# Performance work log

Hardware: AMD Instinct MI355X
Metric: run time of the kernel (lower is better)

The kernel has to match this reference:

```python
import math
import jax, jax.numpy as jnp
import numpy as np

LAM = 1.0
TAU = 0.5
MOM = 0.1
INV_LAM = 1.0 / LAM
E = math.e


def lambertw0(z):
    """Principal branch W0(z) for z >= -1/e via series init + Halley iterations."""
    # init near branch point -1/e: W0 ~ -1 + p - p^2/3 + 11 p^3/72, p = sqrt(2(e z + 1))
    p = jnp.sqrt(jnp.maximum(2.0 * (E * z + 1.0), 0.0))
    w_small = -1.0 + p * (1.0 + p * (-1.0 / 3.0 + p * (11.0 / 72.0)))
    w_big = jnp.log1p(z)  # decent init for z >= 0
    w = jnp.where(z < 0.25, w_small, w_big)
    for _ in range(6):  # Halley's method, quadratic+ convergence
        ew = jnp.exp(w)
        f = w * ew - z
        wp1 = w + 1.0
        denom = ew * wp1 - (w + 2.0) * f / (2.0 * wp1)
        w = w - f / denom
    return w


def setup_inputs() -> dict:
    key = jax.random.key(0)
    loss = jax.random.uniform(key, (33554432,), dtype=jnp.float32)
    return {"loss": loss}


def reference(loss):
    # compute_sigma operates on detached loss -> stop_gradient
    l = jax.lax.stop_gradient(loss)
    tau = (1.0 - MOM) * TAU + MOM * jnp.mean(l)  # running-average tau update
    beta = (l - tau) * INV_LAM
    z = 0.5 * jnp.maximum(-2.0 * math.exp(-1.0), beta)
    sigma = jnp.exp(-lambertw0(z))
    superloss = sigma * loss
    return superloss, sigma
```

## Files before the change

### kernel.cpp

```cpp
#include <hip/hip_runtime.h>


#define NEG_2_OVER_E (-0.73575888234288464320f)

__global__ void __launch_bounds__(256) sum_kernel(const float* __restrict__ loss,
                                                  double* __restrict__ sum_out, int n) {
    int tid = blockIdx.x * blockDim.x + threadIdx.x;
    int stride = gridDim.x * blockDim.x;
    const float4* l4 = (const float4*)loss;
    int n4 = n >> 2;
    float s = 0.0f;
    for (int i = tid; i < n4; i += stride) {
        float4 v = l4[i];
        s += (v.x + v.y) + (v.z + v.w);
    }
    #pragma unroll
    for (int off = 32; off > 0; off >>= 1)
        s += __shfl_down(s, off, 64);
    __shared__ float wsum[4];
    int lane = threadIdx.x & 63;
    int wave = threadIdx.x >> 6;
    if (lane == 0) wsum[wave] = s;
    __syncthreads();
    if (threadIdx.x == 0) {
        float tot = (wsum[0] + wsum[1]) + (wsum[2] + wsum[3]);
        atomicAdd(sum_out, (double)tot);
    }
}

__device__ __forceinline__ float w0_fast(float z) {
    float w = z * fmaf(z, fmaf(z, fmaf(z, fmaf(z, 5.2083333f, -2.6666667f),
                                       1.5f), -1.0f), 1.0f);
    #pragma unroll
    for (int it = 0; it < 2; ++it) {
        float ew = __expf(w);
        float f = fmaf(w, ew, -z);
        float wp1 = w + 1.0f;
        float denom = fmaf(2.0f * ew, wp1 * wp1, -(w + 2.0f) * f);
        w = fmaf(-2.0f * f * wp1, __builtin_amdgcn_rcpf(denom), w);
    }
    return w;
}

__device__ __forceinline__ float sigma_of(float l, float tau) {
    float beta = l - tau;
    float z = 0.5f * fmaxf(NEG_2_OVER_E, beta);
    return __expf(-w0_fast(z));
}

__global__ void __launch_bounds__(256) superloss_kernel(const float* __restrict__ loss,
                                                        float* __restrict__ out,
                                                        const double* __restrict__ sum_ptr,
                                                        int n) {
    int i = blockIdx.x * blockDim.x + threadIdx.x;
    int n4 = n >> 2;
    if (i >= n4) return;

    float mean = (float)(*sum_ptr) * (1.0f / 33554432.0f);
    if (n != 33554432) mean = (float)(*sum_ptr) / (float)n;
    float tau = fmaf(0.1f, mean, 0.45f);

    const float4* l4 = (const float4*)loss;
    float4* sl4 = (float4*)out;
    float4* sg4 = (float4*)(out + n);

    float4 l = l4[i];
    float4 sg, sl;
    sg.x = sigma_of(l.x, tau);
    sg.y = sigma_of(l.y, tau);
    sg.z = sigma_of(l.z, tau);
    sg.w = sigma_of(l.w, tau);
    sl.x = sg.x * l.x;
    sl.y = sg.y * l.y;
    sl.z = sg.z * l.z;
    sl.w = sg.w * l.w;
    sl4[i] = sl;
    sg4[i] = sg;
}

extern "C" void kernel_launch(void* const* d_in, const int* in_sizes, int n_in,
                              void* d_out, int out_size, void* d_ws, size_t ws_size,
                              hipStream_t stream) {
    const float* loss = (const float*)d_in[0];
    int n = in_sizes[0];
    float* out = (float*)d_out;
    double* sum_ws = (double*)d_ws;

    hipMemsetAsync(d_ws, 0, sizeof(double), stream);

    sum_kernel<<<2048, 256, 0, stream>>>(loss, sum_ws, n);

    int n4 = n >> 2;
    int blocks = (n4 + 255) / 256;
    superloss_kernel<<<blocks, 256, 0, stream>>>(loss, out, sum_ws, n);
}
```

Before: 386.3 us.

## Fuse mean reduction and superloss into one cooperative kernel with grid sync

Replaces the memset, sum kernel and elementwise kernel with a single cooperative kernel. Each block writes a partial sum, the grid synchronizes, every block reduces the partials deterministically, and then all blocks compute sigma and superloss in a grid-stride loop. Outputs are written with nontemporal stores. This removes the memset, the double atomics and the launch gaps, but depends on cooperative launch (with a two-kernel fallback) and on a grid-wide barrier. The second read of the 128MB input may or may not hit in cache.

```diff
diff --git a/kernel.cpp b/kernel.cpp
--- a/kernel.cpp
+++ b/kernel.cpp
@@ -1,32 +1,14 @@
 #include <hip/hip_runtime.h>
+#include <hip/hip_cooperative_groups.h>
+
+namespace cg = cooperative_groups;
 
 
 #define NEG_2_OVER_E (-0.73575888234288464320f)
+#define GRID_BLOCKS 1024
+#define BLOCK_THREADS 256
 
-__global__ void __launch_bounds__(256) sum_kernel(const float* __restrict__ loss,
-                                                  double* __restrict__ sum_out, int n) {
-    int tid = blockIdx.x * blockDim.x + threadIdx.x;
-    int stride = gridDim.x * blockDim.x;
-    const float4* l4 = (const float4*)loss;
-    int n4 = n >> 2;
-    float s = 0.0f;
-    for (int i = tid; i < n4; i += stride) {
-        float4 v = l4[i];
-        s += (v.x + v.y) + (v.z + v.w);
-    }
-    #pragma unroll
-    for (int off = 32; off > 0; off >>= 1)
-        s += __shfl_down(s, off, 64);
-    __shared__ float wsum[4];
-    int lane = threadIdx.x & 63;
-    int wave = threadIdx.x >> 6;
-    if (lane == 0) wsum[wave] = s;
-    __syncthreads();
-    if (threadIdx.x == 0) {
-        float tot = (wsum[0] + wsum[1]) + (wsum[2] + wsum[3]);
-        atomicAdd(sum_out, (double)tot);
-    }
-}
+typedef float fx4 __attribute__((ext_vector_type(4)));
 
 __device__ __forceinline__ float w0_fast(float z) {
     float w = z * fmaf(z, fmaf(z, fmaf(z, fmaf(z, 5.2083333f, -2.6666667f),
@@ -48,24 +30,118 @@
     return __expf(-w0_fast(z));
 }
 
-__global__ void __launch_bounds__(256) superloss_kernel(const float* __restrict__ loss,
-                                                        float* __restrict__ out,
-                                                        const double* __restrict__ sum_ptr,
-                                                        int n) {
-    int i = blockIdx.x * blockDim.x + threadIdx.x;
-    int n4 = n >> 2;
+__global__ void __launch_bounds__(BLOCK_THREADS, 4)
+fused_kernel(const float* __restrict__ loss, float* __restrict__ out,
+             float* __restrict__ partials, int n) {
+    const int tid = blockIdx.x * blockDim.x + threadIdx.x;
+    const int nthreads = gridDim.x * blockDim.x;
+    const int n4 = n >> 2;
+    const fx4* l4 = (const fx4*)loss;
+
+    float s = 0.0f;
+    for (int i = tid; i < n4; i += nthreads) {
+        fx4 v = l4[i];
+        s += (v.x + v.y) + (v.z + v.w);
+    }
+    #pragma unroll
+    for (int off = 32; off > 0; off >>= 1)
+        s += __shfl_down(s, off, 64);
+    __shared__ float wsum[4];
+    const int lane = threadIdx.x & 63;
+    const int wave = threadIdx.x >> 6;
+    if (lane == 0) wsum[wave] = s;
+    __syncthreads();
+    if (threadIdx.x == 0)
+        partials[blockIdx.x] = (wsum[0] + wsum[1]) + (wsum[2] + wsum[3]);
+
+    __threadfence();
+    cg::this_grid().sync();
+
+    double t = 0.0;
+    for (int i = threadIdx.x; i < gridDim.x; i += blockDim.x)
+        t += (double)partials[i];
+    #pragma unroll
+    for (int off = 32; off > 0; off >>= 1)
+        t += __shfl_down(t, off, 64);
+    __shared__ double wsumd[4];
+    if (lane == 0) wsumd[wave] = t;
+    __syncthreads();
+    const double total = (wsumd[0] + wsumd[1]) + (wsumd[2] + wsumd[3]);
+    const float mean = (float)(total / (double)n);
+    const float tau = fmaf(0.1f, mean, 0.45f);
+
+    fx4* sl4 = (fx4*)out;
+    fx4* sg4 = (fx4*)(out + n);
+    for (int i = tid; i < n4; i += nthreads) {
+        fx4 l = l4[i];
+        fx4 sg, sl;
+        sg.x = sigma_of(l.x, tau);
+        sg.y = sigma_of(l.y, tau);
+        sg.z = sigma_of(l.z, tau);
+        sg.w = sigma_of(l.w, tau);
+        sl.x = sg.x * l.x;
+        sl.y = sg.y * l.y;
+        sl.z = sg.z * l.z;
+        sl.w = sg.w * l.w;
+        __builtin_nontemporal_store(sl, &sl4[i]);
+        __builtin_nontemporal_store(sg, &sg4[i]);
+    }
+    const int tail = n & 3;
+    if (tail && blockIdx.x == 0 && threadIdx.x < tail) {
+        const int idx = (n4 << 2) + threadIdx.x;
+        float l = loss[idx];
+        float sg = sigma_of(l, tau);
+        out[idx] = sg * l;
+        out[n + idx] = sg;
+    }
+}
+
+__global__ void __launch_bounds__(BLOCK_THREADS) sum_kernel_fb(const float* __restrict__ loss,
+                                                               float* __restrict__ partials, int n) {
+    const int tid = blockIdx.x * blockDim.x + threadIdx.x;
+    const int stride = gridDim.x * blockDim.x;
+    const fx4* l4 = (const fx4*)loss;
+    const int n4 = n >> 2;
+    float s = 0.0f;
+    for (int i = tid; i < n4; i += stride) {
+        fx4 v = l4[i];
+        s += (v.x + v.y) + (v.z + v.w);
+    }
+    #pragma unroll
+    for (int off = 32; off > 0; off >>= 1)
+        s += __shfl_down(s, off, 64);
+    __shared__ float wsum[4];
+    if ((threadIdx.x & 63) == 0) wsum[threadIdx.x >> 6] = s;
+    __syncthreads();
+    if (threadIdx.x == 0)
+        partials[blockIdx.x] = (wsum[0] + wsum[1]) + (wsum[2] + wsum[3]);
+}
+
+__global__ void __launch_bounds__(BLOCK_THREADS) superloss_kernel_fb(const float* __restrict__ loss,
+                                                                     float* __restrict__ out,
+                                                                     const float* __restrict__ partials,
+                                                                     int nparts, int n) {
+    double t = 0.0;
+    for (int i = threadIdx.x; i < nparts; i += blockDim.x)
+        t += (double)partials[i];
+    #pragma unroll
+    for (int off = 32; off > 0; off >>= 1)
+        t += __shfl_down(t, off, 64);
+    __shared__ double wsumd[4];
+    if ((threadIdx.x & 63) == 0) wsumd[threadIdx.x >> 6] = t;
+    __syncthreads();
+    const double total = (wsumd[0] + wsumd[1]) + (wsumd[2] + wsumd[3]);
+    const float mean = (float)(total / (double)n);
+    const float tau = fmaf(0.1f, mean, 0.45f);
+
+    const int i = blockIdx.x * blockDim.x + threadIdx.x;
+    const int n4 = n >> 2;
     if (i >= n4) return;
-
-    float mean = (float)(*sum_ptr) * (1.0f / 33554432.0f);
-    if (n != 33554432) mean = (float)(*sum_ptr) / (float)n;
-    float tau = fmaf(0.1f, mean, 0.45f);
-
-    const float4* l4 = (const float4*)loss;
-    float4* sl4 = (float4*)out;
-    float4* sg4 = (float4*)(out + n);
-
-    float4 l = l4[i];
-    float4 sg, sl;
+    const fx4* l4 = (const fx4*)loss;
+    fx4* sl4 = (fx4*)out;
+    fx4* sg4 = (fx4*)(out + n);
+    fx4 l = l4[i];
+    fx4 sg, sl;
     sg.x = sigma_of(l.x, tau);
     sg.y = sigma_of(l.y, tau);
     sg.z = sigma_of(l.z, tau);
@@ -74,8 +150,8 @@
     sl.y = sg.y * l.y;
     sl.z = sg.z * l.z;
     sl.w = sg.w * l.w;
-    sl4[i] = sl;
-    sg4[i] = sg;
+    __builtin_nontemporal_store(sl, &sl4[i]);
+    __builtin_nontemporal_store(sg, &sg4[i]);
 }
 
 extern "C" void kernel_launch(void* const* d_in, const int* in_sizes, int n_in,
@@ -84,13 +160,17 @@
     const float* loss = (const float*)d_in[0];
     int n = in_sizes[0];
     float* out = (float*)d_out;
-    double* sum_ws = (double*)d_ws;
+    float* partials = (float*)d_ws;
 
-    hipMemsetAsync(d_ws, 0, sizeof(double), stream);
-
-    sum_kernel<<<2048, 256, 0, stream>>>(loss, sum_ws, n);
-
-    int n4 = n >> 2;
-    int blocks = (n4 + 255) / 256;
-    superloss_kernel<<<blocks, 256, 0, stream>>>(loss, out, sum_ws, n);
+    void* args[] = {(void*)&loss, (void*)&out, (void*)&partials, (void*)&n};
+    hipError_t err = hipLaunchCooperativeKernel((const void*)fused_kernel,
+                                                dim3(GRID_BLOCKS), dim3(BLOCK_THREADS),
+                                                args, 0, stream);
+    if (err != hipSuccess) {
+        int nparts = GRID_BLOCKS;
+        sum_kernel_fb<<<GRID_BLOCKS, BLOCK_THREADS, 0, stream>>>(loss, partials, n);
+        int n4 = n >> 2;
+        int blocks = (n4 + BLOCK_THREADS - 1) / BLOCK_THREADS;
+        superloss_kernel_fb<<<blocks, BLOCK_THREADS, 0, stream>>>(loss, out, partials, nparts, n);
+    }
 }
```

New measurement: 488.6 us. +26.5%, slower.
